# Performance work log

Hardware: AMD Instinct MI355X
Metric: run time of the kernel (lower is better)

The kernel has to match this reference:

```python
import jax, jax.numpy as jnp
import numpy as np

B, T, M, H = 256, 64, 256, 256


def setup_inputs() -> dict:
    key = jax.random.key(0)
    ks = jax.random.split(key, 16)
    n = jax.random.normal
    s = 0.05  # small init so tanh/sigmoid stay in sane range
    return {
        "enc_inputs": n(ks[0], (T, B, M), jnp.float32),  # module transposes (0,1) itself
        "y": n(ks[1], (B, T, 1), jnp.float32),
        "W_d": n(ks[2], (M, 2 * H), jnp.float32) * s,
        "b_Wd": n(ks[3], (M,), jnp.float32) * s,
        "U_d": n(ks[4], (M, M), jnp.float32) * s,
        "v_d": n(ks[5], (1, M), jnp.float32) * s,
        "w_tilda": n(ks[6], (1, M + 1), jnp.float32) * s,
        "b_wt": n(ks[7], (1,), jnp.float32) * s,
        "W_ih": n(ks[8], (4 * H, 1), jnp.float32) * s,
        "W_hh": n(ks[9], (4 * H, H), jnp.float32) * s,
        "b_ih": n(ks[10], (4 * H,), jnp.float32) * s,
        "b_hh": n(ks[11], (4 * H,), jnp.float32) * s,
        "W_y": n(ks[12], (H, H + M), jnp.float32) * s,
        "b_Wy": n(ks[13], (H,), jnp.float32) * s,
        "v_y": n(ks[14], (1, H), jnp.float32) * s,
        "b_vy": n(ks[15], (1,), jnp.float32) * s,
    }


def reference(enc_inputs, y, W_d, b_Wd, U_d, v_d, w_tilda, b_wt,
              W_ih, W_hh, b_ih, b_hh, W_y, b_Wy, v_y, b_vy):
    enc = jnp.swapaxes(enc_inputs, 0, 1)                 # (B,T,M)
    # U_d(enc) is loop-invariant; hoist (same math as recomputing per step)
    y1 = jnp.einsum('btm,nm->btn', enc, U_d)             # (B,T,M)
    ys = jnp.swapaxes(y, 0, 1)                           # (T,B,1) scanned over time
    b = enc.shape[0]
    d0 = jnp.zeros((b, H), enc.dtype)
    s0 = jnp.zeros((b, H), enc.dtype)
    c0 = jnp.zeros((b, M), enc.dtype)

    def step(carry, y_t):
        d, sp, _ = carry
        # Bahdanau-style temporal attention over encoder steps
        x1 = jnp.concatenate([d, sp], axis=1) @ W_d.T + b_Wd      # (B,M)
        l = jnp.tanh(x1[:, None, :] + y1) @ v_d[0]                # (B,T)
        beta = jax.nn.softmax(l, axis=1)
        c = jnp.einsum('bt,btm->bm', beta, enc)                   # (B,M)
        # scalar driving input for the decoder LSTM cell
        y_til = jnp.concatenate([c, y_t], axis=1) @ w_tilda.T + b_wt  # (B,1)
        # torch.nn.LSTMCell update with (h, c) = (d, sp)
        gates = y_til @ W_ih.T + b_ih + d @ W_hh.T + b_hh         # (B,4H)
        i, f, g, o = jnp.split(gates, 4, axis=1)
        sp_new = jax.nn.sigmoid(f) * sp + jax.nn.sigmoid(i) * jnp.tanh(g)
        d_new = jax.nn.sigmoid(o) * jnp.tanh(sp_new)
        return (d_new, sp_new, c), None

    (d, sp, c), _ = jax.lax.scan(step, (d0, s0, c0), ys)
    h = jnp.concatenate([d, c], axis=1) @ W_y.T + b_Wy            # (B,H)
    return h @ v_y.T + b_vy                                        # (B,1)
```

## Files before the change

### kernel.cpp

```cpp
#include <hip/hip_runtime.h>


#define Bx 256
#define Tx 64
#define Mx 256
#define Hx 256
#define NT 1024
#define XS 20

typedef unsigned int  uint;
typedef unsigned short ushort;
typedef _Float16 h2  __attribute__((ext_vector_type(2)));
typedef float    f2v __attribute__((ext_vector_type(2)));

__device__ __forceinline__ float4 ld4(const float* p) { return *(const float4*)p; }
__device__ __forceinline__ float h2f(ushort s) {
  union { ushort s; _Float16 h; } c; c.s = s; return (float)c.h;
}
__device__ __forceinline__ ushort f2h(float f) {
  union { _Float16 h; ushort s; } c; c.h = (_Float16)f; return c.s;
}
__device__ __forceinline__ uint pk2(float a, float b) {
  return (uint)f2h(a) | ((uint)f2h(b) << 16);
}

#if defined(__has_builtin)
#if __has_builtin(__builtin_amdgcn_rcpf)
#define RCPF(x) __builtin_amdgcn_rcpf(x)
#endif
#if __has_builtin(__builtin_amdgcn_fdot2)
#define HAVE_FDOT2 1
#endif
#if __has_builtin(__builtin_amdgcn_cvt_pk_f32_fp8) && __has_builtin(__builtin_amdgcn_cvt_pk_fp8_f32)
#define HAVE_FP8 1
#endif
#endif
#ifndef RCPF
#define RCPF(x) (1.0f / (x))
#endif

__device__ __forceinline__ float tanh_fast(float x) {
  float e2 = __expf(2.0f * x);
  return 1.0f - 2.0f * RCPF(e2 + 1.0f);
}
__device__ __forceinline__ float sigm(float x) {
  return RCPF(1.0f + __expf(-x));
}
__device__ __forceinline__ float wave_sum(float v) {
  #pragma unroll
  for (int o = 1; o < 64; o <<= 1) v += __shfl_xor(v, o, 64);
  return v;
}
__device__ __forceinline__ int xsw(int m) { return (m >> 4) * XS + (m & 15); }

__device__ __forceinline__ float dot2u(uint w, uint a, float acc) {
#ifdef HAVE_FDOT2
  h2 W = __builtin_bit_cast(h2, w);
  h2 A = __builtin_bit_cast(h2, a);
  return __builtin_amdgcn_fdot2(W, A, acc, false);
#else
  return acc + h2f((ushort)w) * h2f((ushort)a)
             + h2f((ushort)(w >> 16)) * h2f((ushort)(a >> 16));
#endif
}

__device__ __forceinline__ uint sw8(float f) {
  union { float f; uint u; } c; c.f = f;
  uint s = (c.u >> 31) << 7;
  float a = fabsf(f);
  if (!(a >= 0.0009765625f)) return s;
  if (a >= 448.f) return s | 0x7e;
  int e = (int)((c.u >> 23) & 0xff) - 127;
  if (e < -6) { int q = (int)(a * 512.f + 0.5f); return s | (uint)q; }
  uint m = ((c.u & 0x7fffff) + 0x80000) >> 20;
  if (m == 8) { m = 0; ++e; }
  if (e > 8) return s | 0x7e;
  return s | ((uint)(e + 7) << 3) | m;
}
__device__ __forceinline__ float sw8d(uint b) {
  uint s = b >> 7, e = (b >> 3) & 0xf, m = b & 7;
  float v;
  if (e) { union { uint u; float f; } c; c.u = ((e + 120u) << 23) | (m << 20); v = c.f; }
  else v = (float)m * 0.001953125f;
  return s ? -v : v;
}
__device__ __forceinline__ uint pk_fp8x4(float w0, float w1, float w2, float w3) {
#ifdef HAVE_FP8
  int u = 0;
  u = __builtin_amdgcn_cvt_pk_fp8_f32(w0, w1, u, false);
  u = __builtin_amdgcn_cvt_pk_fp8_f32(w2, w3, u, true);
  return (uint)u;
#else
  return sw8(w0) | (sw8(w1) << 8) | (sw8(w2) << 16) | (sw8(w3) << 24);
#endif
}
template <bool HI>
__device__ __forceinline__ f2v dec2(uint w) {
#ifdef HAVE_FP8
  return __builtin_amdgcn_cvt_pk_f32_fp8((int)w, HI);
#else
  uint b0 = HI ? ((w >> 16) & 0xffu) : (w & 0xffu);
  uint b1 = HI ? (w >> 24) : ((w >> 8) & 0xffu);
  return f2v{sw8d(b0), sw8d(b1)};
#endif
}
__device__ __forceinline__ f2v dotq(uint w, float4 a, f2v acc) {
  acc += dec2<false>(w) * f2v{a.x, a.y};
  acc += dec2<true>(w)  * f2v{a.z, a.w};
  return acc;
}

__global__ __launch_bounds__(256)
void pack_weights(const float* __restrict__ W_d,
                  const float* __restrict__ W_hh,
                  const float* __restrict__ U_d,
                  const float* __restrict__ W_y,
                  uint4* __restrict__ Whh8q,
                  uint4* __restrict__ Wd8q,
                  uint4* __restrict__ Ud8,
                  float* __restrict__ Wyt) {
  const int blk = blockIdx.x, tid = threadIdx.x;
  if (blk < 16) {
    const int k16 = blk;
    #pragma unroll
    for (int q = 0; q < 4; ++q) {
      const int j = tid + 256 * q;
      const float* wr = W_hh + (size_t)j * 256 + 16 * k16;
      float4 a = ld4(wr), b = ld4(wr + 4), c = ld4(wr + 8), d = ld4(wr + 12);
      uint4 u;
      u.x = pk_fp8x4(16.f * a.x, 16.f * a.y, 16.f * a.z, 16.f * a.w);
      u.y = pk_fp8x4(16.f * b.x, 16.f * b.y, 16.f * b.z, 16.f * b.w);
      u.z = pk_fp8x4(16.f * c.x, 16.f * c.y, 16.f * c.z, 16.f * c.w);
      u.w = pk_fp8x4(16.f * d.x, 16.f * d.y, 16.f * d.z, 16.f * d.w);
      Whh8q[k16 * 1024 + j] = u;
    }
  } else if (blk < 48) {
    const int k16 = blk - 16;
    const float* wr = W_d + (size_t)tid * 512 + 16 * k16;
    float4 a = ld4(wr), b = ld4(wr + 4), c = ld4(wr + 8), d = ld4(wr + 12);
    uint4 u;
    u.x = pk_fp8x4(16.f * a.x, 16.f * a.y, 16.f * a.z, 16.f * a.w);
    u.y = pk_fp8x4(16.f * b.x, 16.f * b.y, 16.f * b.z, 16.f * b.w);
    u.z = pk_fp8x4(16.f * c.x, 16.f * c.y, 16.f * c.z, 16.f * c.w);
    u.w = pk_fp8x4(16.f * d.x, 16.f * d.y, 16.f * d.z, 16.f * d.w);
    Wd8q[k16 * 256 + tid] = u;
  } else if (blk < 80) {
    const int m8 = blk - 48;
    float4 a = ld4(U_d + (size_t)tid * 256 + 8 * m8);
    float4 b = ld4(U_d + (size_t)tid * 256 + 8 * m8 + 4);
    Ud8[m8 * 256 + tid] = uint4{pk2(a.x, a.y), pk2(a.z, a.w),
                                pk2(b.x, b.y), pk2(b.z, b.w)};
  } else {
    const int k0 = (blk - 80) * 4;
    float4 w = ld4(W_y + (size_t)tid * 512 + k0);
    Wyt[(k0 + 0) * 256 + tid] = w.x;
    Wyt[(k0 + 1) * 256 + tid] = w.y;
    Wyt[(k0 + 2) * 256 + tid] = w.z;
    Wyt[(k0 + 3) * 256 + tid] = w.w;
  }
}

__global__ __launch_bounds__(NT, 1)
void fused(const float* __restrict__ enc,
           const float* __restrict__ yv,
           const float* __restrict__ b_Wd,
           const float* __restrict__ v_d,
           const float* __restrict__ w_tilda,
           const float* __restrict__ b_wt,
           const float* __restrict__ W_ih,
           const float* __restrict__ b_ih,
           const float* __restrict__ b_hh,
           const float* __restrict__ b_Wy,
           const float* __restrict__ v_y,
           const float* __restrict__ b_vy,
           const uint4* __restrict__ Whh8q,
           const uint4* __restrict__ Wd8q,
           const uint4* __restrict__ Ud8,
           const float* __restrict__ Wyt,
           ushort* __restrict__ Y1,
           float* __restrict__ out)
{
  extern __shared__ __align__(16) uint4 wdl[];
  __shared__ __align__(16) float dsp_s[2 * Hx];
  __shared__ __align__(16) float xq_s[2 * 16 * XS];
  __shared__ __align__(16) float vd_s[16 * XS];
  __shared__ float gates_s[1024];
  __shared__ float dcfin_s[2 * Hx];
  __shared__ float l_s[Tx];
  __shared__ uint  beta2_s[Tx / 2];
  __shared__ float e_s[Tx];
  __shared__ float red_s[4];
  __shared__ float ytil_s;
  __shared__ unsigned flagX, flagL;

  const int b   = blockIdx.x;
  const int tid = threadIdx.x;
  const int h   = tid & 255;
  const int p   = tid >> 8;
  const size_t BM = (size_t)Bx * Mx;

  #pragma unroll
  for (int i = 0; i < 8; ++i) wdl[i * NT + tid] = Wd8q[i * NT + tid];
  if (tid < 256) vd_s[xsw(tid)] = v_d[tid];
  if (tid < 512) dsp_s[tid] = 0.0f;
  if (tid == 0) { flagX = 0u; flagL = 0u; }

  float bj0 = 0.f, bj1 = 0.f;
  if (tid < 512) { bj0 = b_ih[tid] + b_hh[tid]; bj1 = b_ih[tid + 512] + b_hh[tid + 512]; }
  float bWd_r = 0.f;
  if (tid >= 512 && tid < 768) bWd_r = b_Wd[tid - 512];
  float wih0 = 0.f, wih1 = 0.f, wih2 = 0.f, wih3 = 0.f;
  if (tid >= 512 && tid < 768) {
    const int hh = tid - 512;
    wih0 = W_ih[hh]; wih1 = W_ih[hh + 256]; wih2 = W_ih[hh + 512]; wih3 = W_ih[hh + 768];
  }
  float yv_r = 0.f;
  if (tid >= 512 && tid < 576) yv_r = yv[b * Tx + (tid - 512)];
  const float wty = w_tilda[Mx];
  const float bwt = b_wt[0];

  if (tid < Tx) {
    const float* er = enc + (size_t)tid * BM + (size_t)b * Mx;
    float acc = 0.0f;
    for (int m = 0; m < Mx; m += 4) {
      float4 e4 = ld4(er + m);
      float4 w4 = ld4(w_tilda + m);
      acc += e4.x * w4.x + e4.y * w4.y + e4.z * w4.z + e4.w * w4.w;
    }
    e_s[tid] = acc;
  }

  {
    const int n = h;
    const float* eb = enc + (size_t)b * Mx;
    for (int tb = p * 16; tb < p * 16 + 16; tb += 8) {
      f2v acc2[8];
      #pragma unroll
      for (int j = 0; j < 8; ++j) acc2[j] = f2v{0.f, 0.f};
      #pragma unroll 2
      for (int m8 = 0; m8 < 32; ++m8) {
        uint4 u = Ud8[m8 * 256 + n];
        f2v w01 = f2v{h2f((ushort)u.x), h2f((ushort)(u.x >> 16))};
        f2v w23 = f2v{h2f((ushort)u.y), h2f((ushort)(u.y >> 16))};
        f2v w45 = f2v{h2f((ushort)u.z), h2f((ushort)(u.z >> 16))};
        f2v w67 = f2v{h2f((ushort)u.w), h2f((ushort)(u.w >> 16))};
        #pragma unroll
        for (int j = 0; j < 8; ++j) {
          const float* ep = eb + (size_t)(tb + j) * BM + 8 * m8;
          float4 ea = ld4(ep), eb4 = ld4(ep + 4);
          acc2[j] += f2v{ea.x, ea.y} * w01;
          acc2[j] += f2v{ea.z, ea.w} * w23;
          acc2[j] += f2v{eb4.x, eb4.y} * w45;
          acc2[j] += f2v{eb4.z, eb4.w} * w67;
        }
      }
      #pragma unroll
      for (int j = 0; j < 8; ++j)
        Y1[((size_t)b * Tx + tb + j) * Mx + n] = f2h(acc2[j].x + acc2[j].y);
    }
  }
  __syncthreads();

  float sp_reg = 0.0f;

  for (int t = 0; t < Tx; ++t) {
    if (tid < 512) {
      f2v ga = f2v{0.f, 0.f}, gb = f2v{0.f, 0.f};
      const uint4* wp = Whh8q + tid;
      #pragma unroll 2
      for (int c = 0; c < 16; ++c) {
        uint4 wa = wp[c * 1024];
        uint4 wb = wp[c * 1024 + 512];
        const float4* ap = (const float4*)dsp_s + 4 * c;
        float4 a0 = ap[0], a1 = ap[1], a2 = ap[2], a3 = ap[3];
        ga = dotq(wa.x, a0, ga); ga = dotq(wa.y, a1, ga);
        ga = dotq(wa.z, a2, ga); ga = dotq(wa.w, a3, ga);
        gb = dotq(wb.x, a0, gb); gb = dotq(wb.y, a1, gb);
        gb = dotq(wb.z, a2, gb); gb = dotq(wb.w, a3, gb);
      }
      gates_s[tid]       = (ga.x + ga.y) * 0.0625f + bj0;
      gates_s[tid + 512] = (gb.x + gb.y) * 0.0625f + bj1;
    } else {
      const int idx = tid - 512;
      const int m = idx & 255, q = idx >> 8;
      const int tq = idx >> 3, lq = idx & 7;
      const ushort* y1r = Y1 + ((size_t)b * Tx + tq) * Mx + lq * 32;
      uint4 yq0 = *(const uint4*)(y1r);
      uint4 yq1 = *(const uint4*)(y1r + 8);
      uint4 yq2 = *(const uint4*)(y1r + 16);
      uint4 yq3 = *(const uint4*)(y1r + 24);
      {
        f2v xa2 = f2v{0.f, 0.f};
        const uint4* xp = wdl + m + (q * 16) * 256;
        #pragma unroll 4
        for (int i = 0; i < 16; ++i) {
          uint4 u = xp[i * 256];
          const float4* ap = (const float4*)dsp_s + 64 * q + 4 * i;
          float4 a0 = ap[0], a1 = ap[1], a2 = ap[2], a3 = ap[3];
          xa2 = dotq(u.x, a0, xa2); xa2 = dotq(u.y, a1, xa2);
          xa2 = dotq(u.z, a2, xa2); xa2 = dotq(u.w, a3, xa2);
        }
        xq_s[q * (16 * XS) + xsw(m)] = (xa2.x + xa2.y) * 0.0625f
                                     + (q == 0 ? bWd_r : 0.0f);
      }
      __threadfence_block();
      if ((threadIdx.x & 63) == 0)
        __hip_atomic_fetch_add(&flagX, 1u, __ATOMIC_RELEASE, __HIP_MEMORY_SCOPE_WORKGROUP);
      const unsigned tgtX = 8u * (unsigned)(t + 1);
      while (__hip_atomic_load(&flagX, __ATOMIC_ACQUIRE, __HIP_MEMORY_SCOPE_WORKGROUP) < tgtX) {}

      {
        float ps = 0.0f;
        uint yy[8] = {yq0.x, yq0.y, yq0.z, yq0.w, yq1.x, yq1.y, yq1.z, yq1.w};
        uint zz[8] = {yq2.x, yq2.y, yq2.z, yq2.w, yq3.x, yq3.y, yq3.z, yq3.w};
        #pragma unroll
        for (int g = 0; g < 8; ++g) {
          const int c   = 2 * lq + (g >> 2);
          const int off = c * XS + 4 * (g & 3);
          float4 xa0 = *(const float4*)(xq_s + off);
          float4 xa1 = *(const float4*)(xq_s + 16 * XS + off);
          float4 vv  = *(const float4*)(vd_s + off);
          uint ya = (g < 4) ? yy[2 * g] : zz[2 * (g - 4)];
          uint yb = (g < 4) ? yy[2 * g + 1] : zz[2 * (g - 4) + 1];
          ps += tanh_fast(xa0.x + xa1.x + h2f((ushort)ya)) * vv.x
              + tanh_fast(xa0.y + xa1.y + h2f((ushort)(ya >> 16))) * vv.y
              + tanh_fast(xa0.z + xa1.z + h2f((ushort)yb)) * vv.z
              + tanh_fast(xa0.w + xa1.w + h2f((ushort)(yb >> 16))) * vv.w;
        }
        ps += __shfl_xor(ps, 1, 64);
        ps += __shfl_xor(ps, 2, 64);
        ps += __shfl_xor(ps, 4, 64);
        if (lq == 0) l_s[tq] = ps;
      }
      __threadfence_block();
      if ((threadIdx.x & 63) == 0)
        __hip_atomic_fetch_add(&flagL, 1u, __ATOMIC_RELEASE, __HIP_MEMORY_SCOPE_WORKGROUP);

      if (idx < 64) {
        const unsigned tgtL = 8u * (unsigned)(t + 1);
        while (__hip_atomic_load(&flagL, __ATOMIC_ACQUIRE, __HIP_MEMORY_SCOPE_WORKGROUP) < tgtL) {}
        float e0  = __expf(l_s[idx]);
        float den = e0;
        float num = e0 * e_s[idx];
        #pragma unroll
        for (int o = 1; o < 64; o <<= 1) {
          den += __shfl_xor(den, o, 64);
          num += __shfl_xor(num, o, 64);
        }
        if (t == Tx - 1) {
          float beta = e0 * RCPF(den);
          float bn = __shfl_xor(beta, 1, 64);
          if (!(idx & 1)) beta2_s[idx >> 1] = pk2(beta, bn);
        }
        if (idx == t) ytil_s = num * RCPF(den) + wty * yv_r + bwt;
      }
    }
    __syncthreads();

    if (tid >= 512 && tid < 768) {
      const int hh = tid - 512;
      const float ytil = ytil_s;
      float fi = sigm(gates_s[hh]       + ytil * wih0);
      float ff = sigm(gates_s[256 + hh] + ytil * wih1);
      float fg = tanh_fast(gates_s[512 + hh] + ytil * wih2);
      float fo = sigm(gates_s[768 + hh] + ytil * wih3);
      float spn = ff * sp_reg + fi * fg;
      float dn  = fo * tanh_fast(spn);
      sp_reg = spn;
      dsp_s[hh]       = dn;
      dsp_s[256 + hh] = spn;
      if (t == Tx - 1) dcfin_s[hh] = dn;
    }
    __syncthreads();
  }

  if (tid >= 512) {
    const int idx = tid - 512;
    const int m = idx >> 1, q = idx & 1;
    float acc = 0.0f;
    #pragma unroll 4
    for (int j = 0; j < 32; ++j) {
      const int tt = q * 32 + j;
      uint bp = beta2_s[tt >> 1];
      float bb = (tt & 1) ? h2f((ushort)(bp >> 16)) : h2f((ushort)bp);
      acc += bb * enc[(size_t)tt * BM + (size_t)b * Mx + m];
    }
    acc += __shfl_xor(acc, 1, 64);
    if (q == 0) dcfin_s[256 + m] = acc;
  }
  __syncthreads();

  {
    float a = 0.0f;
    const float* wy = Wyt + h;
    for (int k = 128 * p; k < 128 * p + 128; ++k)
      a += wy[(size_t)k * 256] * dcfin_s[k];
    gates_s[p * 256 + h] = a;
  }
  __syncthreads();
  if (tid < 256) {
    float aa = gates_s[h] + gates_s[256 + h] + gates_s[512 + h] + gates_s[768 + h]
             + b_Wy[h];
    float po = aa * v_y[h];
    po = wave_sum(po);
    if ((tid & 63) == 0) red_s[tid >> 6] = po;
  }
  __syncthreads();
  if (tid == 0) out[b] = red_s[0] + red_s[1] + red_s[2] + red_s[3] + b_vy[0];
}

extern "C" void kernel_launch(void* const* d_in, const int* in_sizes, int n_in,
                              void* d_out, int out_size, void* d_ws, size_t ws_size,
                              hipStream_t stream) {
  const float* enc     = (const float*)d_in[0];
  const float* yv      = (const float*)d_in[1];
  const float* W_d     = (const float*)d_in[2];
  const float* b_Wd    = (const float*)d_in[3];
  const float* U_d     = (const float*)d_in[4];
  const float* v_d     = (const float*)d_in[5];
  const float* w_tilda = (const float*)d_in[6];
  const float* b_wt    = (const float*)d_in[7];
  const float* W_ih    = (const float*)d_in[8];
  const float* W_hh    = (const float*)d_in[9];
  const float* b_ih    = (const float*)d_in[10];
  const float* b_hh    = (const float*)d_in[11];
  const float* W_y     = (const float*)d_in[12];
  const float* b_Wy    = (const float*)d_in[13];
  const float* v_y     = (const float*)d_in[14];
  const float* b_vy    = (const float*)d_in[15];
  float* outp = (float*)d_out;

  char* ws = (char*)d_ws;
  uint4* Whh8q = (uint4*)ws;
  uint4* Wd8q  = (uint4*)(ws + (256 << 10));
  uint4* Ud8   = (uint4*)(ws + (384 << 10));
  float* Wyt   = (float*)(ws + (512 << 10));
  ushort* Y1   = (ushort*)(ws + (1024 << 10));

  const int DYN_LDS = 128 << 10;
  hipFuncSetAttribute((const void*)fused,
                      hipFuncAttributeMaxDynamicSharedMemorySize, DYN_LDS);

  hipLaunchKernelGGL(pack_weights, dim3(208), dim3(256), 0, stream,
                     W_d, W_hh, U_d, W_y, Whh8q, Wd8q, Ud8, Wyt);
  hipLaunchKernelGGL(fused, dim3(Bx), dim3(NT), DYN_LDS, stream,
                     enc, yv, b_Wd, v_d, w_tilda, b_wt, W_ih, b_ih, b_hh,
                     b_Wy, v_y, b_vy, Whh8q, Wd8q, Ud8, Wyt, Y1, outp);
}
```

Baseline: 600.9 us.

## Hoist Y1 into registers, prefetch Whh weights, pre-scale tanh inputs, add priorities

The Y1 slice each thread needs is loaded into registers once before the time loop, instead of being reloaded from global memory every step. The Whh8q weight loads are software-pipelined two iterations ahead. U_d and b_Wd are pre-scaled by 2 so the attention tanh skips one multiply per element. The change also adds s_sleep in the spin-wait, raises wave priority on the critical softmax and LSTM paths, and changes launch bounds from (NT,1) to (NT,4). The launch-bounds change may force a tighter register budget, which could cause spills given the extra 16 held registers and the prefetch buffers.

```diff
diff --git a/kernel.cpp b/kernel.cpp
--- a/kernel.cpp
+++ b/kernel.cpp
@@ -43,6 +43,9 @@
   float e2 = __expf(2.0f * x);
   return 1.0f - 2.0f * RCPF(e2 + 1.0f);
 }
+__device__ __forceinline__ float tanh_pre(float z2) {
+  return 1.0f - 2.0f * RCPF(__expf(z2) + 1.0f);
+}
 __device__ __forceinline__ float sigm(float x) {
   return RCPF(1.0f + __expf(-x));
 }
@@ -52,17 +55,6 @@
   return v;
 }
 __device__ __forceinline__ int xsw(int m) { return (m >> 4) * XS + (m & 15); }
-
-__device__ __forceinline__ float dot2u(uint w, uint a, float acc) {
-#ifdef HAVE_FDOT2
-  h2 W = __builtin_bit_cast(h2, w);
-  h2 A = __builtin_bit_cast(h2, a);
-  return __builtin_amdgcn_fdot2(W, A, acc, false);
-#else
-  return acc + h2f((ushort)w) * h2f((ushort)a)
-             + h2f((ushort)(w >> 16)) * h2f((ushort)(a >> 16));
-#endif
-}
 
 __device__ __forceinline__ uint sw8(float f) {
   union { float f; uint u; } c; c.f = f;
@@ -148,8 +140,8 @@
     const int m8 = blk - 48;
     float4 a = ld4(U_d + (size_t)tid * 256 + 8 * m8);
     float4 b = ld4(U_d + (size_t)tid * 256 + 8 * m8 + 4);
-    Ud8[m8 * 256 + tid] = uint4{pk2(a.x, a.y), pk2(a.z, a.w),
-                                pk2(b.x, b.y), pk2(b.z, b.w)};
+    Ud8[m8 * 256 + tid] = uint4{pk2(2.f * a.x, 2.f * a.y), pk2(2.f * a.z, 2.f * a.w),
+                                pk2(2.f * b.x, 2.f * b.y), pk2(2.f * b.z, 2.f * b.w)};
   } else {
     const int k0 = (blk - 80) * 4;
     float4 w = ld4(W_y + (size_t)tid * 512 + k0);
@@ -160,7 +152,7 @@
   }
 }
 
-__global__ __launch_bounds__(NT, 1)
+__global__ __launch_bounds__(NT, 4)
 void fused(const float* __restrict__ enc,
            const float* __restrict__ yv,
            const float* __restrict__ b_Wd,
@@ -208,7 +200,7 @@
   float bj0 = 0.f, bj1 = 0.f;
   if (tid < 512) { bj0 = b_ih[tid] + b_hh[tid]; bj1 = b_ih[tid + 512] + b_hh[tid + 512]; }
   float bWd_r = 0.f;
-  if (tid >= 512 && tid < 768) bWd_r = b_Wd[tid - 512];
+  if (tid >= 512 && tid < 768) bWd_r = 2.0f * b_Wd[tid - 512];
   float wih0 = 0.f, wih1 = 0.f, wih2 = 0.f, wih3 = 0.f;
   if (tid >= 512 && tid < 768) {
     const int hh = tid - 512;
@@ -261,16 +253,37 @@
   }
   __syncthreads();
 
+  uint yreg[16];
+  #pragma unroll
+  for (int i = 0; i < 16; ++i) yreg[i] = 0u;
+  float e_r = 0.0f;
+  if (tid >= 512) {
+    const int idx = tid - 512;
+    const int tq = idx >> 3, lq = idx & 7;
+    const ushort* y1r = Y1 + ((size_t)b * Tx + tq) * Mx + lq * 32;
+    uint4 a = *(const uint4*)(y1r);
+    uint4 b4 = *(const uint4*)(y1r + 8);
+    uint4 c4 = *(const uint4*)(y1r + 16);
+    uint4 d4 = *(const uint4*)(y1r + 24);
+    yreg[0] = a.x;  yreg[1] = a.y;  yreg[2] = a.z;  yreg[3] = a.w;
+    yreg[4] = b4.x; yreg[5] = b4.y; yreg[6] = b4.z; yreg[7] = b4.w;
+    yreg[8] = c4.x; yreg[9] = c4.y; yreg[10] = c4.z; yreg[11] = c4.w;
+    yreg[12] = d4.x; yreg[13] = d4.y; yreg[14] = d4.z; yreg[15] = d4.w;
+    if (idx < 64) e_r = e_s[idx];
+  }
+
   float sp_reg = 0.0f;
 
   for (int t = 0; t < Tx; ++t) {
     if (tid < 512) {
+      const uint4* wp = Whh8q + tid;
+      uint4 pa = wp[0],    pb = wp[512];
+      uint4 qa = wp[1024], qb = wp[1024 + 512];
       f2v ga = f2v{0.f, 0.f}, gb = f2v{0.f, 0.f};
-      const uint4* wp = Whh8q + tid;
-      #pragma unroll 2
+      #pragma unroll
       for (int c = 0; c < 16; ++c) {
-        uint4 wa = wp[c * 1024];
-        uint4 wb = wp[c * 1024 + 512];
+        uint4 wa = pa, wb = pb; pa = qa; pb = qb;
+        if (c < 14) { qa = wp[(c + 2) * 1024]; qb = wp[(c + 2) * 1024 + 512]; }
         const float4* ap = (const float4*)dsp_s + 4 * c;
         float4 a0 = ap[0], a1 = ap[1], a2 = ap[2], a3 = ap[3];
         ga = dotq(wa.x, a0, ga); ga = dotq(wa.y, a1, ga);
@@ -284,11 +297,6 @@
       const int idx = tid - 512;
       const int m = idx & 255, q = idx >> 8;
       const int tq = idx >> 3, lq = idx & 7;
-      const ushort* y1r = Y1 + ((size_t)b * Tx + tq) * Mx + lq * 32;
-      uint4 yq0 = *(const uint4*)(y1r);
-      uint4 yq1 = *(const uint4*)(y1r + 8);
-      uint4 yq2 = *(const uint4*)(y1r + 16);
-      uint4 yq3 = *(const uint4*)(y1r + 24);
       {
         f2v xa2 = f2v{0.f, 0.f};
         const uint4* xp = wdl + m + (q * 16) * 256;
@@ -300,19 +308,18 @@
           xa2 = dotq(u.x, a0, xa2); xa2 = dotq(u.y, a1, xa2);
           xa2 = dotq(u.z, a2, xa2); xa2 = dotq(u.w, a3, xa2);
         }
-        xq_s[q * (16 * XS) + xsw(m)] = (xa2.x + xa2.y) * 0.0625f
+        xq_s[q * (16 * XS) + xsw(m)] = (xa2.x + xa2.y) * 0.125f
                                      + (q == 0 ? bWd_r : 0.0f);
       }
       __threadfence_block();
       if ((threadIdx.x & 63) == 0)
         __hip_atomic_fetch_add(&flagX, 1u, __ATOMIC_RELEASE, __HIP_MEMORY_SCOPE_WORKGROUP);
       const unsigned tgtX = 8u * (unsigned)(t + 1);
-      while (__hip_atomic_load(&flagX, __ATOMIC_ACQUIRE, __HIP_MEMORY_SCOPE_WORKGROUP) < tgtX) {}
+      while (__hip_atomic_load(&flagX, __ATOMIC_ACQUIRE, __HIP_MEMORY_SCOPE_WORKGROUP) < tgtX)
+        __builtin_amdgcn_s_sleep(1);
 
       {
         float ps = 0.0f;
-        uint yy[8] = {yq0.x, yq0.y, yq0.z, yq0.w, yq1.x, yq1.y, yq1.z, yq1.w};
-        uint zz[8] = {yq2.x, yq2.y, yq2.z, yq2.w, yq3.x, yq3.y, yq3.z, yq3.w};
         #pragma unroll
         for (int g = 0; g < 8; ++g) {
           const int c   = 2 * lq + (g >> 2);
@@ -320,12 +327,11 @@
           float4 xa0 = *(const float4*)(xq_s + off);
           float4 xa1 = *(const float4*)(xq_s + 16 * XS + off);
           float4 vv  = *(const float4*)(vd_s + off);
-          uint ya = (g < 4) ? yy[2 * g] : zz[2 * (g - 4)];
-          uint yb = (g < 4) ? yy[2 * g + 1] : zz[2 * (g - 4) + 1];
-          ps += tanh_fast(xa0.x + xa1.x + h2f((ushort)ya)) * vv.x
-              + tanh_fast(xa0.y + xa1.y + h2f((ushort)(ya >> 16))) * vv.y
-              + tanh_fast(xa0.z + xa1.z + h2f((ushort)yb)) * vv.z
-              + tanh_fast(xa0.w + xa1.w + h2f((ushort)(yb >> 16))) * vv.w;
+          uint ya = yreg[2 * g], yb = yreg[2 * g + 1];
+          ps += tanh_pre(xa0.x + xa1.x + h2f((ushort)ya)) * vv.x
+              + tanh_pre(xa0.y + xa1.y + h2f((ushort)(ya >> 16))) * vv.y
+              + tanh_pre(xa0.z + xa1.z + h2f((ushort)yb)) * vv.z
+              + tanh_pre(xa0.w + xa1.w + h2f((ushort)(yb >> 16))) * vv.w;
         }
         ps += __shfl_xor(ps, 1, 64);
         ps += __shfl_xor(ps, 2, 64);
@@ -337,11 +343,12 @@
         __hip_atomic_fetch_add(&flagL, 1u, __ATOMIC_RELEASE, __HIP_MEMORY_SCOPE_WORKGROUP);
 
       if (idx < 64) {
+        __builtin_amdgcn_s_setprio(1);
         const unsigned tgtL = 8u * (unsigned)(t + 1);
         while (__hip_atomic_load(&flagL, __ATOMIC_ACQUIRE, __HIP_MEMORY_SCOPE_WORKGROUP) < tgtL) {}
         float e0  = __expf(l_s[idx]);
         float den = e0;
-        float num = e0 * e_s[idx];
+        float num = e0 * e_r;
         #pragma unroll
         for (int o = 1; o < 64; o <<= 1) {
           den += __shfl_xor(den, o, 64);
@@ -353,11 +360,13 @@
           if (!(idx & 1)) beta2_s[idx >> 1] = pk2(beta, bn);
         }
         if (idx == t) ytil_s = num * RCPF(den) + wty * yv_r + bwt;
+        __builtin_amdgcn_s_setprio(0);
       }
     }
     __syncthreads();
 
     if (tid >= 512 && tid < 768) {
+      __builtin_amdgcn_s_setprio(1);
       const int hh = tid - 512;
       const float ytil = ytil_s;
       float fi = sigm(gates_s[hh]       + ytil * wih0);
@@ -370,6 +379,7 @@
       dsp_s[hh]       = dn;
       dsp_s[256 + hh] = spn;
       if (t == Tx - 1) dcfin_s[hh] = dn;
+      __builtin_amdgcn_s_setprio(0);
     }
     __syncthreads();
   }
```

New measurement: 736.4 us. 1.23x slower.
